# Kernel tuning notes

Hardware: AMD Instinct MI355X
Metric: run time of the kernel (lower is better)

Reference implementation:

```python
import jax, jax.numpy as jnp
import numpy as np

N = 8192
F_IN = 512
F_HID = 256
ALPHA = 0.2  # LeakyReLU negative slope
NEG_INF = -9e15


def gat_layer(h, adj, W, a):
    """Standard dense GraphAttentionLayer (pyGAT style).
    h: [N, F_in], adj: [N, N] (0/1), W: [F_in, F_out], a: [2*F_out, 1].
    """
    Wh = h @ W  # [N, F_out]
    f_out = W.shape[1]
    # e_ij = leakyrelu(a1 . Wh_i + a2 . Wh_j) via broadcasting
    e1 = Wh @ a[:f_out]      # [N, 1]
    e2 = Wh @ a[f_out:]      # [N, 1]
    e = jax.nn.leaky_relu(e1 + e2.T, negative_slope=ALPHA)  # [N, N]
    e = jnp.where(adj > 0, e, NEG_INF)
    att = jax.nn.softmax(e, axis=-1)  # masked row softmax
    return jax.nn.elu(att @ Wh)       # [N, F_out]


def setup_inputs() -> dict:
    key = jax.random.key(0)
    k_x, k_adj, k_w1, k_a1, k_w2, k_a2 = jax.random.split(key, 6)
    x = jax.random.normal(k_x, (N, F_IN), dtype=jnp.float32)
    # sparse random adjacency (~avg degree 16) + self loops
    adj = (jax.random.uniform(k_adj, (N, N)) < (16.0 / N)).astype(jnp.float32)
    adj = jnp.clip(adj + jnp.eye(N, dtype=jnp.float32), 0.0, 1.0)
    # Xavier-ish init for layer params
    W1 = jax.random.normal(k_w1, (F_IN, F_HID), dtype=jnp.float32) * (1.0 / np.sqrt(F_IN))
    a1 = jax.random.normal(k_a1, (2 * F_HID, 1), dtype=jnp.float32) * (1.0 / np.sqrt(2 * F_HID))
    W2 = jax.random.normal(k_w2, (F_HID, F_IN), dtype=jnp.float32) * (1.0 / np.sqrt(F_HID))
    a2 = jax.random.normal(k_a2, (2 * F_IN, 1), dtype=jnp.float32) * (1.0 / np.sqrt(2 * F_IN))
    return {"x": x, "adj": adj, "W1": W1, "a1": a1, "W2": W2, "a2": a2}


def reference(x, adj, W1, a1, W2, a2):
    enc = gat_layer(x, adj, W1, a1)    # encode: [N, F_HID]
    dec = gat_layer(enc, adj, W2, a2)  # decode: [N, F_IN]
    return (dec, enc)
```

## Files before the change

kernel.cpp:

```cpp
#include <hip/hip_runtime.h>
#include <hip/hip_bf16.h>

#define N_NODES 8192
#define F_IN    512
#define F_HID   256
#define ALPHA   0.2f
#define MAXDEG  64

using f32x4 = __attribute__((ext_vector_type(4))) float;
using f16x8 = __attribute__((ext_vector_type(8))) _Float16;
using f16x4 = __attribute__((ext_vector_type(4))) _Float16;

__global__ void conv_WT(const float* __restrict__ W1, const float* __restrict__ W2,
                        _Float16* __restrict__ W1T, _Float16* __restrict__ W2T,
                        float* __restrict__ stz) {
    int gid = blockIdx.x * blockDim.x + threadIdx.x;
    if (gid < 4 * N_NODES) stz[gid] = 0.0f;

    int t = blockIdx.x;
    const float* W; _Float16* WT; int K, N, kt, nt;
    if (t < 128) { W = W1; WT = W1T; K = 512; N = 256; kt = t & 15; nt = t >> 4; }
    else { t -= 128; W = W2; WT = W2T; K = 256; N = 512; kt = t & 7; nt = t >> 3; }
    __shared__ float Ws[32][33];
    const int tx = threadIdx.x & 31, ty = threadIdx.x >> 5;
    #pragma unroll
    for (int i = 0; i < 4; ++i)
        Ws[ty + 8 * i][tx] = W[(size_t)(kt * 32 + ty + 8 * i) * N + nt * 32 + tx];
    __syncthreads();
    #pragma unroll
    for (int i = 0; i < 4; ++i)
        WT[(size_t)(nt * 32 + ty + 8 * i) * K + kt * 32 + tx] = (_Float16)Ws[tx][ty + 8 * i];
}

__device__ inline void csr_row(const float* __restrict__ adj, int* __restrict__ cols,
                               int* __restrict__ cnt, int row, int lane) {
    const f32x4* arow = (const f32x4*)(adj + (size_t)row * N_NODES);
    int* crow = cols + (size_t)row * MAXDEG;
    int count = 0;
    const unsigned long long mlt = (1ULL << lane) - 1ULL;
    for (int base = 0; base < N_NODES; base += 512) {
        f32x4 v0 = __builtin_nontemporal_load(&arow[(base >> 2) + lane]);
        f32x4 v1 = __builtin_nontemporal_load(&arow[(base >> 2) + 64 + lane]);
        unsigned long long b0 = __ballot(v0[0] > 0.0f);
        unsigned long long b1 = __ballot(v0[1] > 0.0f);
        unsigned long long b2 = __ballot(v0[2] > 0.0f);
        unsigned long long b3 = __ballot(v0[3] > 0.0f);
        unsigned long long b4 = __ballot(v1[0] > 0.0f);
        unsigned long long b5 = __ballot(v1[1] > 0.0f);
        unsigned long long b6 = __ballot(v1[2] > 0.0f);
        unsigned long long b7 = __ballot(v1[3] > 0.0f);
        int o = count + __popcll(b0 & mlt) + __popcll(b1 & mlt)
                      + __popcll(b2 & mlt) + __popcll(b3 & mlt);
        int c0 = base + (lane << 2);
        if (v0[0] > 0.0f) { if (o < MAXDEG) crow[o] = c0;     o++; }
        if (v0[1] > 0.0f) { if (o < MAXDEG) crow[o] = c0 + 1; o++; }
        if (v0[2] > 0.0f) { if (o < MAXDEG) crow[o] = c0 + 2; o++; }
        if (v0[3] > 0.0f) { if (o < MAXDEG) crow[o] = c0 + 3; o++; }
        count += __popcll(b0) + __popcll(b1) + __popcll(b2) + __popcll(b3);
        o = count + __popcll(b4 & mlt) + __popcll(b5 & mlt)
                  + __popcll(b6 & mlt) + __popcll(b7 & mlt);
        int c1 = base + 256 + (lane << 2);
        if (v1[0] > 0.0f) { if (o < MAXDEG) crow[o] = c1;     o++; }
        if (v1[1] > 0.0f) { if (o < MAXDEG) crow[o] = c1 + 1; o++; }
        if (v1[2] > 0.0f) { if (o < MAXDEG) crow[o] = c1 + 2; o++; }
        if (v1[3] > 0.0f) { if (o < MAXDEG) crow[o] = c1 + 3; o++; }
        count += __popcll(b4) + __popcll(b5) + __popcll(b6) + __popcll(b7);
    }
    if (lane == 0) cnt[row] = count > MAXDEG ? MAXDEG : count;
}

__device__ inline void gemm1_tile(const float* __restrict__ x,
                                  const _Float16* __restrict__ W1T,
                                  _Float16* __restrict__ Wh1,
                                  const float* __restrict__ a1,
                                  float* __restrict__ s1, float* __restrict__ t1,
                                  int brow, int bcol) {
    const int LDT = 72;
    __shared__ _Float16 As[64 * LDT];
    __shared__ _Float16 Bs[64 * LDT];
    const int tid = threadIdx.x;
    const int wid = tid >> 6, lane = tid & 63;
    const int wr = (wid >> 1) * 32, wc = (wid & 1) * 32;
    const int sr = tid >> 3, skg = (tid & 7) * 8;

    f32x4 acc[2][2];
    #pragma unroll
    for (int m = 0; m < 2; ++m)
        #pragma unroll
        for (int n = 0; n < 2; ++n) acc[m][n] = f32x4{0.f, 0.f, 0.f, 0.f};

    for (int k0 = 0; k0 < F_IN; k0 += 64) {
        #pragma unroll
        for (int i = 0; i < 2; ++i) {
            int r = sr + i * 32;
            const f32x4* src = (const f32x4*)(x + (size_t)(brow + r) * F_IN + k0 + skg);
            f32x4 a0 = __builtin_nontemporal_load(src);
            f32x4 a1v = __builtin_nontemporal_load(src + 1);
            f16x8 av;
            #pragma unroll
            for (int j = 0; j < 4; ++j) { av[j] = (_Float16)a0[j]; av[4 + j] = (_Float16)a1v[j]; }
            *(f16x8*)&As[r * LDT + skg] = av;
            *(f16x8*)&Bs[r * LDT + skg] = *(const f16x8*)&W1T[(size_t)(bcol + r) * F_IN + k0 + skg];
        }
        __syncthreads();
        #pragma unroll
        for (int ks = 0; ks < 2; ++ks) {
            const int kb = ks * 32 + (lane >> 4) * 8;
            f16x8 af[2], bfr[2];
            #pragma unroll
            for (int m = 0; m < 2; ++m)
                af[m] = *(const f16x8*)&As[(wr + m * 16 + (lane & 15)) * LDT + kb];
            #pragma unroll
            for (int n = 0; n < 2; ++n)
                bfr[n] = *(const f16x8*)&Bs[(wc + n * 16 + (lane & 15)) * LDT + kb];
            #pragma unroll
            for (int m = 0; m < 2; ++m)
                #pragma unroll
                for (int n = 0; n < 2; ++n)
                    acc[m][n] = __builtin_amdgcn_mfma_f32_16x16x32_f16(
                        af[m], bfr[n], acc[m][n], 0, 0, 0);
        }
        __syncthreads();
    }
    const int c0 = bcol + wc + (lane & 15);
    float as0 = a1[c0],         as1 = a1[c0 + 16];
    float at0 = a1[F_HID + c0], at1 = a1[F_HID + c0 + 16];
    #pragma unroll
    for (int m = 0; m < 2; ++m) {
        #pragma unroll
        for (int j = 0; j < 4; ++j) {
            float vs = acc[m][0][j] * as0 + acc[m][1][j] * as1;
            float vt = acc[m][0][j] * at0 + acc[m][1][j] * at1;
            #pragma unroll
            for (int off = 1; off < 16; off <<= 1) {
                vs += __shfl_xor(vs, off);
                vt += __shfl_xor(vt, off);
            }
            if ((lane & 15) == 0) {
                int row = brow + wr + m * 16 + ((lane >> 4) << 2) + j;
                atomicAdd(s1 + row, vs);
                atomicAdd(t1 + row, vt);
            }
        }
        #pragma unroll
        for (int n = 0; n < 2; ++n) {
            int row = brow + wr + m * 16 + ((lane >> 4) << 2);
            int col = bcol + wc + n * 16 + (lane & 15);
            #pragma unroll
            for (int j = 0; j < 4; ++j)
                Wh1[(size_t)(row + j) * F_HID + col] = (_Float16)acc[m][n][j];
        }
    }
}

__global__ __launch_bounds__(256)
void csr_and_gemm1(const float* __restrict__ adj, int* __restrict__ cols,
                   int* __restrict__ cnt, const float* __restrict__ x,
                   const _Float16* __restrict__ W1T, _Float16* __restrict__ Wh1,
                   const float* __restrict__ a1,
                   float* __restrict__ s1, float* __restrict__ t1) {
    const int bid = blockIdx.x;
    const int g = bid / 5, r = bid % 5;
    if (r == 0) {
        gemm1_tile(x, W1T, Wh1, a1, s1, t1, (g >> 2) * 64, (g & 3) * 64);
    } else {
        const int cb = g * 4 + (r - 1);
        const int row = cb * 4 + (threadIdx.x >> 6);
        csr_row(adj, cols, cnt, row, threadIdx.x & 63);
    }
}

__global__ __launch_bounds__(256)
void gemm2_f16(const _Float16* __restrict__ A, const _Float16* __restrict__ BT,
               _Float16* __restrict__ C, const float* __restrict__ a2,
               float* __restrict__ s2, float* __restrict__ t2) {
    const int LDT = 72, LDB = 264;
    __shared__ _Float16 As[128 * LDT];
    __shared__ _Float16 Bs[64 * LDB];
    const int tid = threadIdx.x;
    const int wid = tid >> 6, lane = tid & 63;
    const int brow = (blockIdx.x >> 3) * 128;
    const int bcol = (blockIdx.x & 7) * 64;
    const int wr = (wid >> 1) * 64, wc = (wid & 1) * 32;

    #pragma unroll
    for (int i = 0; i < 8; ++i) {
        int id = tid + i * 256;
        int r = id >> 5, kc = (id & 31) * 8;
        *(f16x8*)&Bs[r * LDB + kc] = *(const f16x8*)&BT[(size_t)(bcol + r) * F_HID + kc];
    }

    f32x4 acc[4][2];
    #pragma unroll
    for (int m = 0; m < 4; ++m)
        #pragma unroll
        for (int n = 0; n < 2; ++n) acc[m][n] = f32x4{0.f, 0.f, 0.f, 0.f};

    for (int k0 = 0; k0 < F_HID; k0 += 64) {
        #pragma unroll
        for (int i = 0; i < 4; ++i) {
            int id = tid + i * 256;
            int r = id >> 3, kc = (id & 7) * 8;
            *(f16x8*)&As[r * LDT + kc] = *(const f16x8*)&A[(size_t)(brow + r) * F_HID + k0 + kc];
        }
        __syncthreads();
        #pragma unroll
        for (int ks = 0; ks < 2; ++ks) {
            const int kb = ks * 32 + (lane >> 4) * 8;
            f16x8 af[4], bfr[2];
            #pragma unroll
            for (int m = 0; m < 4; ++m)
                af[m] = *(const f16x8*)&As[(wr + m * 16 + (lane & 15)) * LDT + kb];
            #pragma unroll
            for (int n = 0; n < 2; ++n)
                bfr[n] = *(const f16x8*)&Bs[(wc + n * 16 + (lane & 15)) * LDB + k0 + kb];
            #pragma unroll
            for (int m = 0; m < 4; ++m)
                #pragma unroll
                for (int n = 0; n < 2; ++n)
                    acc[m][n] = __builtin_amdgcn_mfma_f32_16x16x32_f16(
                        af[m], bfr[n], acc[m][n], 0, 0, 0);
        }
        __syncthreads();
    }
    const int c0 = bcol + wc + (lane & 15);
    float as0 = a2[c0],        as1 = a2[c0 + 16];
    float at0 = a2[F_IN + c0], at1 = a2[F_IN + c0 + 16];
    #pragma unroll
    for (int m = 0; m < 4; ++m) {
        #pragma unroll
        for (int j = 0; j < 4; ++j) {
            float vs = acc[m][0][j] * as0 + acc[m][1][j] * as1;
            float vt = acc[m][0][j] * at0 + acc[m][1][j] * at1;
            #pragma unroll
            for (int off = 1; off < 16; off <<= 1) {
                vs += __shfl_xor(vs, off);
                vt += __shfl_xor(vt, off);
            }
            if ((lane & 15) == 0) {
                int row = brow + wr + m * 16 + ((lane >> 4) << 2) + j;
                atomicAdd(s2 + row, vs);
                atomicAdd(t2 + row, vt);
            }
        }
        #pragma unroll
        for (int n = 0; n < 2; ++n) {
            int row = brow + wr + m * 16 + ((lane >> 4) << 2);
            int col = bcol + wc + n * 16 + (lane & 15);
            #pragma unroll
            for (int j = 0; j < 4; ++j)
                C[(size_t)(row + j) * F_IN + col] = (_Float16)acc[m][n][j];
        }
    }
}

template<int F>
__global__ void aggregate16(const _Float16* __restrict__ Wh,
                            const int* __restrict__ cols, const int* __restrict__ cnt,
                            const float* __restrict__ s, const float* __restrict__ t,
                            float* __restrict__ out, _Float16* __restrict__ out16) {
    const int EL = F / 64;
    const int wid = threadIdx.x >> 6, lane = threadIdx.x & 63;
    const int row = blockIdx.x * 4 + wid;
    const int deg = cnt[row];
    __shared__ float pS[4][64];
    __shared__ int jS[4][64];
    int j = 0;
    float ev = -1e30f;
    if (lane < deg) {
        j = cols[(size_t)row * MAXDEG + lane];
        float z = s[row] + t[j];
        ev = z > 0.0f ? z : ALPHA * z;
    }
    float m = ev;
    #pragma unroll
    for (int off = 32; off > 0; off >>= 1) m = fmaxf(m, __shfl_xor(m, off));
    float ex = (lane < deg) ? __expf(ev - m) : 0.0f;
    float sum = ex;
    #pragma unroll
    for (int off = 32; off > 0; off >>= 1) sum += __shfl_xor(sum, off);
    pS[wid][lane] = ex / sum;
    jS[wid][lane] = j;
    __syncthreads();

    float acc[EL] = {};
    const size_t lo = (size_t)lane * EL;
    int d = 0;
    for (; d + 8 <= deg; d += 8) {
        float p[8]; const _Float16* w[8];
        #pragma unroll
        for (int q = 0; q < 8; ++q) {
            p[q] = pS[wid][d + q];
            w[q] = Wh + (size_t)jS[wid][d + q] * F + lo;
        }
        if constexpr (EL == 8) {
            f16x8 v[8];
            #pragma unroll
            for (int q = 0; q < 8; ++q) v[q] = *(const f16x8*)w[q];
            #pragma unroll
            for (int jj = 0; jj < 8; ++jj) {
                float a = 0.f;
                #pragma unroll
                for (int q = 0; q < 8; ++q) a += p[q] * (float)v[q][jj];
                acc[jj] += a;
            }
        } else {
            f16x4 v[8];
            #pragma unroll
            for (int q = 0; q < 8; ++q) v[q] = *(const f16x4*)w[q];
            #pragma unroll
            for (int jj = 0; jj < 4; ++jj) {
                float a = 0.f;
                #pragma unroll
                for (int q = 0; q < 8; ++q) a += p[q] * (float)v[q][jj];
                acc[jj] += a;
            }
        }
    }
    for (; d + 4 <= deg; d += 4) {
        float p0 = pS[wid][d],     p1 = pS[wid][d + 1];
        float p2 = pS[wid][d + 2], p3 = pS[wid][d + 3];
        const _Float16* w0 = Wh + (size_t)jS[wid][d] * F + lo;
        const _Float16* w1 = Wh + (size_t)jS[wid][d + 1] * F + lo;
        const _Float16* w2 = Wh + (size_t)jS[wid][d + 2] * F + lo;
        const _Float16* w3 = Wh + (size_t)jS[wid][d + 3] * F + lo;
        if constexpr (EL == 8) {
            f16x8 v0 = *(const f16x8*)w0, v1 = *(const f16x8*)w1;
            f16x8 v2 = *(const f16x8*)w2, v3 = *(const f16x8*)w3;
            #pragma unroll
            for (int jj = 0; jj < 8; ++jj)
                acc[jj] += p0 * (float)v0[jj] + p1 * (float)v1[jj]
                         + p2 * (float)v2[jj] + p3 * (float)v3[jj];
        } else {
            f16x4 v0 = *(const f16x4*)w0, v1 = *(const f16x4*)w1;
            f16x4 v2 = *(const f16x4*)w2, v3 = *(const f16x4*)w3;
            #pragma unroll
            for (int jj = 0; jj < 4; ++jj)
                acc[jj] += p0 * (float)v0[jj] + p1 * (float)v1[jj]
                         + p2 * (float)v2[jj] + p3 * (float)v3[jj];
        }
    }
    for (; d < deg; ++d) {
        float p = pS[wid][d];
        const _Float16* wr = Wh + (size_t)jS[wid][d] * F + lo;
        if constexpr (EL == 8) {
            f16x8 w = *(const f16x8*)wr;
            #pragma unroll
            for (int jj = 0; jj < 8; ++jj) acc[jj] += p * (float)w[jj];
        } else {
            f16x4 w = *(const f16x4*)wr;
            #pragma unroll
            for (int jj = 0; jj < 4; ++jj) acc[jj] += p * (float)w[jj];
        }
    }
    #pragma unroll
    for (int c = 0; c < EL / 4; ++c) {
        f32x4 o; f16x4 h;
        #pragma unroll
        for (int jj = 0; jj < 4; ++jj) {
            float v = acc[c * 4 + jj];
            float e = v > 0.0f ? v : (__expf(v) - 1.0f);
            o[jj] = e; h[jj] = (_Float16)e;
        }
        __builtin_nontemporal_store(o, (f32x4*)(out + (size_t)row * F + lo + c * 4));
        if (out16)
            *(f16x4*)(out16 + (size_t)row * F + lo + c * 4) = h;
    }
}

extern "C" void kernel_launch(void* const* d_in, const int* in_sizes, int n_in,
                              void* d_out, int out_size, void* d_ws, size_t ws_size,
                              hipStream_t stream) {
    (void)in_sizes; (void)n_in; (void)out_size; (void)ws_size;
    const float* x   = (const float*)d_in[0];
    const float* adj = (const float*)d_in[1];
    const float* W1  = (const float*)d_in[2];
    const float* a1  = (const float*)d_in[3];
    const float* W2  = (const float*)d_in[4];
    const float* a2  = (const float*)d_in[5];

    float* dec = (float*)d_out;
    float* enc = dec + (size_t)N_NODES * F_IN;

    int*      cols  = (int*)d_ws;
    int*      cnt   = cols + (size_t)N_NODES * MAXDEG;
    float*    s1    = (float*)(cnt + N_NODES);
    float*    t1    = s1 + N_NODES;
    float*    s2    = t1 + N_NODES;
    float*    t2    = s2 + N_NODES;
    _Float16* Wh1   = (_Float16*)(t2 + N_NODES);
    _Float16* Wh2   = Wh1 + (size_t)N_NODES * F_HID;
    _Float16* enc16 = Wh2 + (size_t)N_NODES * F_IN;
    _Float16* W1T   = enc16 + (size_t)N_NODES * F_HID;
    _Float16* W2T   = W1T + (size_t)F_HID * F_IN;

    conv_WT<<<256, 256, 0, stream>>>(W1, W2, W1T, W2T, s1);

    csr_and_gemm1<<<2560, 256, 0, stream>>>(adj, cols, cnt, x, W1T, Wh1, a1, s1, t1);

    aggregate16<F_HID><<<N_NODES / 4, 256, 0, stream>>>(Wh1, cols, cnt, s1, t1, enc, enc16);

    gemm2_f16<<<512, 256, 0, stream>>>(enc16, W2T, Wh2, a2, s2, t2);

    aggregate16<F_IN><<<N_NODES / 4, 256, 0, stream>>>(Wh2, cols, cnt, s2, t2, dec, (_Float16*)nullptr);
}
```

Baseline: 114.4 us.

## Reassociate layer-2 as (att·enc)·W2 and fold attention scores into layer-1 epilogue

Layer 2 now aggregates the 256-wide encoder features over neighbours first and then multiplies by W2, instead of computing Wh2 = enc·W2 and gathering 512-wide rows. Attention logits s2/t2 are computed directly from enc using precomputed W2·a2 vectors inside the layer-1 aggregate, which removes the atomics and the intermediate Wh2 buffer. The aim is to halve gather traffic in the second aggregation and drop a 512-wide fp16 intermediate. In exchange it adds an extra fp16 rounding of the aggregated features before the GEMM, and the logits use fp32 enc rather than the fp16-rounded Wh2.

Result: faster. 108.0 us (-5.6%).

```diff
diff --git a/kernel.cpp b/kernel.cpp
--- a/kernel.cpp
+++ b/kernel.cpp
@@ -13,16 +13,36 @@
 
 __global__ void conv_WT(const float* __restrict__ W1, const float* __restrict__ W2,
                         _Float16* __restrict__ W1T, _Float16* __restrict__ W2T,
+                        const float* __restrict__ a2,
+                        float* __restrict__ w2s, float* __restrict__ w2t,
                         float* __restrict__ stz) {
-    int gid = blockIdx.x * blockDim.x + threadIdx.x;
-    if (gid < 4 * N_NODES) stz[gid] = 0.0f;
+    const int tid = threadIdx.x;
+    int gid = blockIdx.x * 256 + tid;
+    if (gid < 2 * N_NODES) stz[gid] = 0.0f;
+
+    if (blockIdx.x >= 256) {
+        const int r = (blockIdx.x - 256) * 64 + (tid >> 2);
+        const int q = tid & 3;
+        float ss = 0.f, tt = 0.f;
+        for (int n = q * 4; n < F_IN; n += 16) {
+            f32x4 w  = *(const f32x4*)&W2[(size_t)r * F_IN + n];
+            f32x4 as = *(const f32x4*)&a2[n];
+            f32x4 at = *(const f32x4*)&a2[F_IN + n];
+            #pragma unroll
+            for (int j = 0; j < 4; ++j) { ss += w[j] * as[j]; tt += w[j] * at[j]; }
+        }
+        ss += __shfl_xor(ss, 1); ss += __shfl_xor(ss, 2);
+        tt += __shfl_xor(tt, 1); tt += __shfl_xor(tt, 2);
+        if (q == 0) { w2s[r] = ss; w2t[r] = tt; }
+        return;
+    }
 
     int t = blockIdx.x;
     const float* W; _Float16* WT; int K, N, kt, nt;
     if (t < 128) { W = W1; WT = W1T; K = 512; N = 256; kt = t & 15; nt = t >> 4; }
     else { t -= 128; W = W2; WT = W2T; K = 256; N = 512; kt = t & 7; nt = t >> 3; }
     __shared__ float Ws[32][33];
-    const int tx = threadIdx.x & 31, ty = threadIdx.x >> 5;
+    const int tx = tid & 31, ty = tid >> 5;
     #pragma unroll
     for (int i = 0; i < 4; ++i)
         Ws[ty + 8 * i][tx] = W[(size_t)(kt * 32 + ty + 8 * i) * N + nt * 32 + tx];
@@ -170,96 +190,12 @@
     }
 }
 
-__global__ __launch_bounds__(256)
-void gemm2_f16(const _Float16* __restrict__ A, const _Float16* __restrict__ BT,
-               _Float16* __restrict__ C, const float* __restrict__ a2,
-               float* __restrict__ s2, float* __restrict__ t2) {
-    const int LDT = 72, LDB = 264;
-    __shared__ _Float16 As[128 * LDT];
-    __shared__ _Float16 Bs[64 * LDB];
-    const int tid = threadIdx.x;
-    const int wid = tid >> 6, lane = tid & 63;
-    const int brow = (blockIdx.x >> 3) * 128;
-    const int bcol = (blockIdx.x & 7) * 64;
-    const int wr = (wid >> 1) * 64, wc = (wid & 1) * 32;
-
-    #pragma unroll
-    for (int i = 0; i < 8; ++i) {
-        int id = tid + i * 256;
-        int r = id >> 5, kc = (id & 31) * 8;
-        *(f16x8*)&Bs[r * LDB + kc] = *(const f16x8*)&BT[(size_t)(bcol + r) * F_HID + kc];
-    }
-
-    f32x4 acc[4][2];
-    #pragma unroll
-    for (int m = 0; m < 4; ++m)
-        #pragma unroll
-        for (int n = 0; n < 2; ++n) acc[m][n] = f32x4{0.f, 0.f, 0.f, 0.f};
-
-    for (int k0 = 0; k0 < F_HID; k0 += 64) {
-        #pragma unroll
-        for (int i = 0; i < 4; ++i) {
-            int id = tid + i * 256;
-            int r = id >> 3, kc = (id & 7) * 8;
-            *(f16x8*)&As[r * LDT + kc] = *(const f16x8*)&A[(size_t)(brow + r) * F_HID + k0 + kc];
-        }
-        __syncthreads();
-        #pragma unroll
-        for (int ks = 0; ks < 2; ++ks) {
-            const int kb = ks * 32 + (lane >> 4) * 8;
-            f16x8 af[4], bfr[2];
-            #pragma unroll
-            for (int m = 0; m < 4; ++m)
-                af[m] = *(const f16x8*)&As[(wr + m * 16 + (lane & 15)) * LDT + kb];
-            #pragma unroll
-            for (int n = 0; n < 2; ++n)
-                bfr[n] = *(const f16x8*)&Bs[(wc + n * 16 + (lane & 15)) * LDB + k0 + kb];
-            #pragma unroll
-            for (int m = 0; m < 4; ++m)
-                #pragma unroll
-                for (int n = 0; n < 2; ++n)
-                    acc[m][n] = __builtin_amdgcn_mfma_f32_16x16x32_f16(
-                        af[m], bfr[n], acc[m][n], 0, 0, 0);
-        }
-        __syncthreads();
-    }
-    const int c0 = bcol + wc + (lane & 15);
-    float as0 = a2[c0],        as1 = a2[c0 + 16];
-    float at0 = a2[F_IN + c0], at1 = a2[F_IN + c0 + 16];
-    #pragma unroll
-    for (int m = 0; m < 4; ++m) {
-        #pragma unroll
-        for (int j = 0; j < 4; ++j) {
-            float vs = acc[m][0][j] * as0 + acc[m][1][j] * as1;
-            float vt = acc[m][0][j] * at0 + acc[m][1][j] * at1;
-            #pragma unroll
-            for (int off = 1; off < 16; off <<= 1) {
-                vs += __shfl_xor(vs, off);
-                vt += __shfl_xor(vt, off);
-            }
-            if ((lane & 15) == 0) {
-                int row = brow + wr + m * 16 + ((lane >> 4) << 2) + j;
-                atomicAdd(s2 + row, vs);
-                atomicAdd(t2 + row, vt);
-            }
-        }
-        #pragma unroll
-        for (int n = 0; n < 2; ++n) {
-            int row = brow + wr + m * 16 + ((lane >> 4) << 2);
-            int col = bcol + wc + n * 16 + (lane & 15);
-            #pragma unroll
-            for (int j = 0; j < 4; ++j)
-                C[(size_t)(row + j) * F_IN + col] = (_Float16)acc[m][n][j];
-        }
-    }
-}
-
-template<int F>
-__global__ void aggregate16(const _Float16* __restrict__ Wh,
-                            const int* __restrict__ cols, const int* __restrict__ cnt,
-                            const float* __restrict__ s, const float* __restrict__ t,
-                            float* __restrict__ out, _Float16* __restrict__ out16) {
-    const int EL = F / 64;
+__global__ void aggregate_l1(const _Float16* __restrict__ Wh,
+                             const int* __restrict__ cols, const int* __restrict__ cnt,
+                             const float* __restrict__ s, const float* __restrict__ t,
+                             const float* __restrict__ w2s, const float* __restrict__ w2t,
+                             float* __restrict__ enc, _Float16* __restrict__ enc16,
+                             float* __restrict__ s2, float* __restrict__ t2) {
     const int wid = threadIdx.x >> 6, lane = threadIdx.x & 63;
     const int row = blockIdx.x * 4 + wid;
     const int deg = cnt[row];
@@ -283,89 +219,169 @@
     jS[wid][lane] = j;
     __syncthreads();
 
-    float acc[EL] = {};
-    const size_t lo = (size_t)lane * EL;
+    float acc[4] = {};
+    const size_t lo = (size_t)lane * 4;
     int d = 0;
-    for (; d + 8 <= deg; d += 8) {
-        float p[8]; const _Float16* w[8];
-        #pragma unroll
-        for (int q = 0; q < 8; ++q) {
-            p[q] = pS[wid][d + q];
-            w[q] = Wh + (size_t)jS[wid][d + q] * F + lo;
-        }
-        if constexpr (EL == 8) {
-            f16x8 v[8];
-            #pragma unroll
-            for (int q = 0; q < 8; ++q) v[q] = *(const f16x8*)w[q];
-            #pragma unroll
-            for (int jj = 0; jj < 8; ++jj) {
-                float a = 0.f;
-                #pragma unroll
-                for (int q = 0; q < 8; ++q) a += p[q] * (float)v[q][jj];
-                acc[jj] += a;
-            }
-        } else {
-            f16x4 v[8];
-            #pragma unroll
-            for (int q = 0; q < 8; ++q) v[q] = *(const f16x4*)w[q];
-            #pragma unroll
-            for (int jj = 0; jj < 4; ++jj) {
-                float a = 0.f;
-                #pragma unroll
-                for (int q = 0; q < 8; ++q) a += p[q] * (float)v[q][jj];
-                acc[jj] += a;
-            }
-        }
-    }
     for (; d + 4 <= deg; d += 4) {
         float p0 = pS[wid][d],     p1 = pS[wid][d + 1];
         float p2 = pS[wid][d + 2], p3 = pS[wid][d + 3];
-        const _Float16* w0 = Wh + (size_t)jS[wid][d] * F + lo;
-        const _Float16* w1 = Wh + (size_t)jS[wid][d + 1] * F + lo;
-        const _Float16* w2 = Wh + (size_t)jS[wid][d + 2] * F + lo;
-        const _Float16* w3 = Wh + (size_t)jS[wid][d + 3] * F + lo;
-        if constexpr (EL == 8) {
-            f16x8 v0 = *(const f16x8*)w0, v1 = *(const f16x8*)w1;
-            f16x8 v2 = *(const f16x8*)w2, v3 = *(const f16x8*)w3;
-            #pragma unroll
-            for (int jj = 0; jj < 8; ++jj)
-                acc[jj] += p0 * (float)v0[jj] + p1 * (float)v1[jj]
-                         + p2 * (float)v2[jj] + p3 * (float)v3[jj];
-        } else {
-            f16x4 v0 = *(const f16x4*)w0, v1 = *(const f16x4*)w1;
-            f16x4 v2 = *(const f16x4*)w2, v3 = *(const f16x4*)w3;
-            #pragma unroll
-            for (int jj = 0; jj < 4; ++jj)
-                acc[jj] += p0 * (float)v0[jj] + p1 * (float)v1[jj]
-                         + p2 * (float)v2[jj] + p3 * (float)v3[jj];
-        }
+        f16x4 v0 = *(const f16x4*)(Wh + (size_t)jS[wid][d] * F_HID + lo);
+        f16x4 v1 = *(const f16x4*)(Wh + (size_t)jS[wid][d + 1] * F_HID + lo);
+        f16x4 v2 = *(const f16x4*)(Wh + (size_t)jS[wid][d + 2] * F_HID + lo);
+        f16x4 v3 = *(const f16x4*)(Wh + (size_t)jS[wid][d + 3] * F_HID + lo);
+        #pragma unroll
+        for (int jj = 0; jj < 4; ++jj)
+            acc[jj] += p0 * (float)v0[jj] + p1 * (float)v1[jj]
+                     + p2 * (float)v2[jj] + p3 * (float)v3[jj];
     }
     for (; d < deg; ++d) {
         float p = pS[wid][d];
-        const _Float16* wr = Wh + (size_t)jS[wid][d] * F + lo;
-        if constexpr (EL == 8) {
-            f16x8 w = *(const f16x8*)wr;
-            #pragma unroll
-            for (int jj = 0; jj < 8; ++jj) acc[jj] += p * (float)w[jj];
-        } else {
-            f16x4 w = *(const f16x4*)wr;
-            #pragma unroll
-            for (int jj = 0; jj < 4; ++jj) acc[jj] += p * (float)w[jj];
-        }
-    }
-    #pragma unroll
-    for (int c = 0; c < EL / 4; ++c) {
-        f32x4 o; f16x4 h;
-        #pragma unroll
-        for (int jj = 0; jj < 4; ++jj) {
-            float v = acc[c * 4 + jj];
-            float e = v > 0.0f ? v : (__expf(v) - 1.0f);
-            o[jj] = e; h[jj] = (_Float16)e;
-        }
-        __builtin_nontemporal_store(o, (f32x4*)(out + (size_t)row * F + lo + c * 4));
-        if (out16)
-            *(f16x4*)(out16 + (size_t)row * F + lo + c * 4) = h;
-    }
+        f16x4 w = *(const f16x4*)(Wh + (size_t)jS[wid][d] * F_HID + lo);
+        #pragma unroll
+        for (int jj = 0; jj < 4; ++jj) acc[jj] += p * (float)w[jj];
+    }
+    f32x4 o; f16x4 h;
+    #pragma unroll
+    for (int jj = 0; jj < 4; ++jj) {
+        float v = acc[jj];
+        float e = v > 0.0f ? v : (__expf(v) - 1.0f);
+        o[jj] = e; h[jj] = (_Float16)e;
+    }
+    __builtin_nontemporal_store(o, (f32x4*)(enc + (size_t)row * F_HID + lo));
+    *(f16x4*)(enc16 + (size_t)row * F_HID + lo) = h;
+
+    f32x4 ws = *(const f32x4*)(w2s + lo);
+    f32x4 wt = *(const f32x4*)(w2t + lo);
+    float ps = 0.f, pt = 0.f;
+    #pragma unroll
+    for (int jj = 0; jj < 4; ++jj) { ps += o[jj] * ws[jj]; pt += o[jj] * wt[jj]; }
+    #pragma unroll
+    for (int off = 32; off > 0; off >>= 1) {
+        ps += __shfl_xor(ps, off);
+        pt += __shfl_xor(pt, off);
+    }
+    if (lane == 0) { s2[row] = ps; t2[row] = pt; }
+}
+
+__global__ void aggregate_l2pre(const _Float16* __restrict__ enc16,
+                                const int* __restrict__ cols, const int* __restrict__ cnt,
+                                const float* __restrict__ s, const float* __restrict__ t,
+                                _Float16* __restrict__ aggE16) {
+    const int wid = threadIdx.x >> 6, lane = threadIdx.x & 63;
+    const int row = blockIdx.x * 4 + wid;
+    const int deg = cnt[row];
+    __shared__ float pS[4][64];
+    __shared__ int jS[4][64];
+    int j = 0;
+    float ev = -1e30f;
+    if (lane < deg) {
+        j = cols[(size_t)row * MAXDEG + lane];
+        float z = s[row] + t[j];
+        ev = z > 0.0f ? z : ALPHA * z;
+    }
+    float m = ev;
+    #pragma unroll
+    for (int off = 32; off > 0; off >>= 1) m = fmaxf(m, __shfl_xor(m, off));
+    float ex = (lane < deg) ? __expf(ev - m) : 0.0f;
+    float sum = ex;
+    #pragma unroll
+    for (int off = 32; off > 0; off >>= 1) sum += __shfl_xor(sum, off);
+    pS[wid][lane] = ex / sum;
+    jS[wid][lane] = j;
+    __syncthreads();
+
+    float acc[4] = {};
+    const size_t lo = (size_t)lane * 4;
+    int d = 0;
+    for (; d + 4 <= deg; d += 4) {
+        float p0 = pS[wid][d],     p1 = pS[wid][d + 1];
+        float p2 = pS[wid][d + 2], p3 = pS[wid][d + 3];
+        f16x4 v0 = *(const f16x4*)(enc16 + (size_t)jS[wid][d] * F_HID + lo);
+        f16x4 v1 = *(const f16x4*)(enc16 + (size_t)jS[wid][d + 1] * F_HID + lo);
+        f16x4 v2 = *(const f16x4*)(enc16 + (size_t)jS[wid][d + 2] * F_HID + lo);
+        f16x4 v3 = *(const f16x4*)(enc16 + (size_t)jS[wid][d + 3] * F_HID + lo);
+        #pragma unroll
+        for (int jj = 0; jj < 4; ++jj)
+            acc[jj] += p0 * (float)v0[jj] + p1 * (float)v1[jj]
+                     + p2 * (float)v2[jj] + p3 * (float)v3[jj];
+    }
+    for (; d < deg; ++d) {
+        float p = pS[wid][d];
+        f16x4 w = *(const f16x4*)(enc16 + (size_t)jS[wid][d] * F_HID + lo);
+        #pragma unroll
+        for (int jj = 0; jj < 4; ++jj) acc[jj] += p * (float)w[jj];
+    }
+    f16x4 h;
+    #pragma unroll
+    for (int jj = 0; jj < 4; ++jj) h[jj] = (_Float16)acc[jj];
+    *(f16x4*)(aggE16 + (size_t)row * F_HID + lo) = h;
+}
+
+__global__ __launch_bounds__(256)
+void gemm2e(const _Float16* __restrict__ A, const _Float16* __restrict__ BT,
+            float* __restrict__ C) {
+    const int LDT = 72, LDB = 264;
+    __shared__ _Float16 As[128 * LDT];
+    __shared__ _Float16 Bs[64 * LDB];
+    const int tid = threadIdx.x;
+    const int wid = tid >> 6, lane = tid & 63;
+    const int brow = (blockIdx.x >> 3) * 128;
+    const int bcol = (blockIdx.x & 7) * 64;
+    const int wr = (wid >> 1) * 64, wc = (wid & 1) * 32;
+
+    #pragma unroll
+    for (int i = 0; i < 8; ++i) {
+        int id = tid + i * 256;
+        int r = id >> 5, kc = (id & 31) * 8;
+        *(f16x8*)&Bs[r * LDB + kc] = *(const f16x8*)&BT[(size_t)(bcol + r) * F_HID + kc];
+    }
+
+    f32x4 acc[4][2];
+    #pragma unroll
+    for (int m = 0; m < 4; ++m)
+        #pragma unroll
+        for (int n = 0; n < 2; ++n) acc[m][n] = f32x4{0.f, 0.f, 0.f, 0.f};
+
+    for (int k0 = 0; k0 < F_HID; k0 += 64) {
+        #pragma unroll
+        for (int i = 0; i < 4; ++i) {
+            int id = tid + i * 256;
+            int r = id >> 3, kc = (id & 7) * 8;
+            *(f16x8*)&As[r * LDT + kc] = *(const f16x8*)&A[(size_t)(brow + r) * F_HID + k0 + kc];
+        }
+        __syncthreads();
+        #pragma unroll
+        for (int ks = 0; ks < 2; ++ks) {
+            const int kb = ks * 32 + (lane >> 4) * 8;
+            f16x8 af[4], bfr[2];
+            #pragma unroll
+            for (int m = 0; m < 4; ++m)
+                af[m] = *(const f16x8*)&As[(wr + m * 16 + (lane & 15)) * LDT + kb];
+            #pragma unroll
+            for (int n = 0; n < 2; ++n)
+                bfr[n] = *(const f16x8*)&Bs[(wc + n * 16 + (lane & 15)) * LDB + k0 + kb];
+            #pragma unroll
+            for (int m = 0; m < 4; ++m)
+                #pragma unroll
+                for (int n = 0; n < 2; ++n)
+                    acc[m][n] = __builtin_amdgcn_mfma_f32_16x16x32_f16(
+                        af[m], bfr[n], acc[m][n], 0, 0, 0);
+        }
+        __syncthreads();
+    }
+    #pragma unroll
+    for (int m = 0; m < 4; ++m)
+        #pragma unroll
+        for (int n = 0; n < 2; ++n) {
+            int row = brow + wr + m * 16 + ((lane >> 4) << 2);
+            int col = bcol + wc + n * 16 + (lane & 15);
+            #pragma unroll
+            for (int j = 0; j < 4; ++j) {
+                float v = acc[m][n][j];
+                float e = v > 0.0f ? v : (__expf(v) - 1.0f);
+                __builtin_nontemporal_store(e, &C[(size_t)(row + j) * F_IN + col]);
+            }
+        }
 }
 
 extern "C" void kernel_launch(void* const* d_in, const int* in_sizes, int n_in,
@@ -382,25 +398,28 @@
     float* dec = (float*)d_out;
     float* enc = dec + (size_t)N_NODES * F_IN;
 
-    int*      cols  = (int*)d_ws;
-    int*      cnt   = cols + (size_t)N_NODES * MAXDEG;
-    float*    s1    = (float*)(cnt + N_NODES);
-    float*    t1    = s1 + N_NODES;
-    float*    s2    = t1 + N_NODES;
-    float*    t2    = s2 + N_NODES;
-    _Float16* Wh1   = (_Float16*)(t2 + N_NODES);
-    _Float16* Wh2   = Wh1 + (size_t)N_NODES * F_HID;
-    _Float16* enc16 = Wh2 + (size_t)N_NODES * F_IN;
-    _Float16* W1T   = enc16 + (size_t)N_NODES * F_HID;
-    _Float16* W2T   = W1T + (size_t)F_HID * F_IN;
-
-    conv_WT<<<256, 256, 0, stream>>>(W1, W2, W1T, W2T, s1);
+    int*      cols   = (int*)d_ws;
+    int*      cnt    = cols + (size_t)N_NODES * MAXDEG;
+    float*    s1     = (float*)(cnt + N_NODES);
+    float*    t1     = s1 + N_NODES;
+    float*    s2     = t1 + N_NODES;
+    float*    t2     = s2 + N_NODES;
+    float*    w2s    = t2 + N_NODES;
+    float*    w2t    = w2s + F_HID;
+    _Float16* Wh1    = (_Float16*)(w2t + F_HID);
+    _Float16* enc16  = Wh1 + (size_t)N_NODES * F_HID;
+    _Float16* aggE16 = enc16 + (size_t)N_NODES * F_HID;
+    _Float16* W1T    = aggE16 + (size_t)N_NODES * F_HID;
+    _Float16* W2T    = W1T + (size_t)F_HID * F_IN;
+
+    conv_WT<<<260, 256, 0, stream>>>(W1, W2, W1T, W2T, a2, w2s, w2t, s1);
 
     csr_and_gemm1<<<2560, 256, 0, stream>>>(adj, cols, cnt, x, W1T, Wh1, a1, s1, t1);
 
-    aggregate16<F_HID><<<N_NODES / 4, 256, 0, stream>>>(Wh1, cols, cnt, s1, t1, enc, enc16);
-
-    gemm2_f16<<<512, 256, 0, stream>>>(enc16, W2T, Wh2, a2, s2, t2);
-
-    aggregate16<F_IN><<<N_NODES / 4, 256, 0, stream>>>(Wh2, cols, cnt, s2, t2, dec, (_Float16*)nullptr);
-}
+    aggregate_l1<<<N_NODES / 4, 256, 0, stream>>>(Wh1, cols, cnt, s1, t1,
+                                                  w2s, w2t, enc, enc16, s2, t2);
+
+    aggregate_l2pre<<<N_NODES / 4, 256, 0, stream>>>(enc16, cols, cnt, s2, t2, aggE16);
+
+    gemm2e<<<512, 256, 0, stream>>>(aggE16, W2T, dec);
+}
```
